# Kernel optimization log

Measured on AMD Instinct MI355X. Metric: run time of the kernel, lower is better.

Reference implementation:

```python
import jax, jax.numpy as jnp
import numpy as np

EPS = 1e-5  # torch BatchNorm1d default eps

# BinActive: sign forward, straight-through estimator backward (grad clipped where |x|>1)
@jax.custom_vjp
def bin_active(x):
    return jnp.sign(x)

def _ba_fwd(x):
    return jnp.sign(x), x

def _ba_bwd(x, g):
    return (g * (jnp.abs(x) <= 1.0).astype(g.dtype),)

bin_active.defvjp(_ba_fwd, _ba_bwd)

# XNOR-style weight binarization: sign(W) * mean(|W|) per output column, STE backward
@jax.custom_vjp
def bin_weight(w):
    alpha = jnp.mean(jnp.abs(w), axis=0, keepdims=True)  # [1, out]
    return jnp.sign(w) * alpha

def _bw_fwd(w):
    alpha = jnp.mean(jnp.abs(w), axis=0, keepdims=True)
    return jnp.sign(w) * alpha, w

def _bw_bwd(w, g):
    return (g * (jnp.abs(w) <= 1.0).astype(g.dtype),)

bin_weight.defvjp(_bw_fwd, _bw_bwd)


def setup_inputs() -> dict:
    key = jax.random.key(0)
    ks = jax.random.split(key, 8)
    N, E, IN, H, OUT = 100000, 1600000, 256, 128, 40
    x = jax.random.normal(ks[0], (N, IN), dtype=jnp.float32)
    edge_index = jax.random.randint(ks[1], (2, E), 0, N, dtype=jnp.int64)
    W0 = jax.random.normal(ks[2], (IN, H), dtype=jnp.float32) * (2.0 / IN) ** 0.5
    b0 = jnp.zeros((H,), dtype=jnp.float32)
    W1 = jax.random.normal(ks[3], (H, H), dtype=jnp.float32) * (2.0 / H) ** 0.5
    b1 = jnp.zeros((H,), dtype=jnp.float32)
    W2 = jax.random.normal(ks[4], (H, OUT), dtype=jnp.float32) * (2.0 / H) ** 0.5
    b2 = jnp.zeros((OUT,), dtype=jnp.float32)
    return {"x": x, "edge_index": edge_index, "W0": W0, "b0": b0,
            "W1": W1, "b1": b1, "W2": W2, "b2": b2}


def reference(x, edge_index, W0, b0, W1, b1, W2, b2):
    n = x.shape[0]
    loop = jnp.arange(n, dtype=edge_index.dtype)
    src = jnp.concatenate([edge_index[0], loop])  # add self loops (GCN norm)
    dst = jnp.concatenate([edge_index[1], loop])
    deg = jax.ops.segment_sum(jnp.ones_like(src, dtype=x.dtype), dst, num_segments=n)
    dinv = jnp.where(deg > 0, deg ** -0.5, 0.0)
    norm = (dinv[src] * dinv[dst])[:, None]  # [E+N, 1]

    # BatchNorm1d(affine=False), training-mode batch statistics (biased var)
    mu = jnp.mean(x, axis=0)
    var = jnp.var(x, axis=0)
    h = (x - mu) * jax.lax.rsqrt(var + EPS)

    for W, b in ((W0, b0), (W1, b1), (W2, b2)):
        h = bin_active(h)                       # sign binarize (dropout skipped: eval)
        h = h @ bin_weight(W)                   # binary-weight linear
        h = jax.ops.segment_sum(h[src] * norm, dst, num_segments=n) + b  # D^-1/2 (A+I) D^-1/2 agg
    return jax.nn.log_softmax(h, axis=1)
```

## Files before the change

### kernel.cpp

```cpp
#include <hip/hip_runtime.h>
#include <math.h>

#define IN_DIM 256
#define HD 128
#define OUT_DIM 40
#define S2_STRIDE 64
#define NB_CS 1024
#define NXCD 8
#define NCHUNK 64
#define NRANGE 8
#define RMAXW 6400

__device__ __forceinline__ int xcc_id() {
    int x;
    asm volatile("s_getreg_b32 %0, hwreg(HW_REG_XCC_ID)" : "=s"(x));
    return x & (NXCD - 1);
}

__global__ __launch_bounds__(256) void k_init(float* muacc8) {
    int i = blockIdx.x * 256 + threadIdx.x;
    if (i < NXCD * 256) muacc8[i] = 0.f;
}

__global__ __launch_bounds__(256) void k_fuse1(const float* __restrict__ x, int N,
                                               float* __restrict__ muacc8,
                                               const int* __restrict__ ei, int E,
                                               unsigned char* __restrict__ cntC,
                                               const float* __restrict__ W0,
                                               const float* __restrict__ W1,
                                               const float* __restrict__ W2,
                                               unsigned long long* W0p,
                                               unsigned long long* W1p,
                                               unsigned long long* W2p,
                                               float* aS0, float* aS1, float* aS2) {
    __shared__ __align__(16) unsigned ldsbuf[RMAXW];
    int b = blockIdx.x, tid = threadIdx.x;
    if (b < NB_CS) {
        float* lds = (float*)ldsbuf;
        size_t F4 = (size_t)N * (IN_DIM / 4);
        size_t stride = (size_t)NB_CS * 256;
        float a0 = 0.f, a1 = 0.f, a2 = 0.f, a3 = 0.f;
        const float4* x4 = (const float4*)x;
        for (size_t i = (size_t)b * 256 + tid; i < F4; i += stride) {
            float4 v = x4[i];
            a0 += v.x; a1 += v.y; a2 += v.z; a3 += v.w;
        }
        lds[tid] = 0.f;
        __syncthreads();
        int c0 = (tid * 4) & 255;
        atomicAdd(&lds[c0], a0);
        atomicAdd(&lds[c0 + 1], a1);
        atomicAdd(&lds[c0 + 2], a2);
        atomicAdd(&lds[c0 + 3], a3);
        __syncthreads();
        int xc = xcc_id();
        __hip_atomic_fetch_add(&muacc8[xc * 256 + tid], lds[tid],
                               __ATOMIC_RELAXED, __HIP_MEMORY_SCOPE_WORKGROUP);
    } else if (b < NB_CS + NCHUNK * NRANGE) {
        int bid2 = b - NB_CS;
        int c = bid2 >> 3, r = bid2 & (NRANGE - 1);
        for (int i = tid; i < RMAXW; i += 256) ldsbuf[i] = 0u;
        __syncthreads();
        int R = (N + NRANGE - 1) / NRANGE;
        int base = r * R;
        int lim = N - base; if (lim > R) lim = R; if (lim < 0) lim = 0;
        int chunk = ((E + NCHUNK - 1) / NCHUNK + 3) & ~3;
        int eBeg = c * chunk, eEnd = E < eBeg + chunk ? E : eBeg + chunk;
        const int* dptr = ei + E;
        int e = eBeg;
        if ((((unsigned)(E + eBeg)) & 3u) == 0 && eBeg < eEnd) {
            int n4 = (eEnd - eBeg) >> 2;
            const int4* d4 = (const int4*)(dptr + eBeg);
            for (int i = tid; i < n4; i += 256) {
                int4 v = d4[i];
                unsigned r0 = (unsigned)(v.x - base);
                unsigned r1 = (unsigned)(v.y - base);
                unsigned r2 = (unsigned)(v.z - base);
                unsigned r3 = (unsigned)(v.w - base);
                if (r0 < (unsigned)lim) atomicAdd(&ldsbuf[r0 >> 1], 1u << (16 * (r0 & 1)));
                if (r1 < (unsigned)lim) atomicAdd(&ldsbuf[r1 >> 1], 1u << (16 * (r1 & 1)));
                if (r2 < (unsigned)lim) atomicAdd(&ldsbuf[r2 >> 1], 1u << (16 * (r2 & 1)));
                if (r3 < (unsigned)lim) atomicAdd(&ldsbuf[r3 >> 1], 1u << (16 * (r3 & 1)));
            }
            e = eBeg + (n4 << 2);
        }
        for (e += tid; e < eEnd; e += 256) {
            unsigned rel = (unsigned)(dptr[e] - base);
            if (rel < (unsigned)lim) atomicAdd(&ldsbuf[rel >> 1], 1u << (16 * (rel & 1)));
        }
        __syncthreads();
        for (int i = tid; i < lim; i += 256) {
            unsigned cv = (ldsbuf[i >> 1] >> (16 * (i & 1))) & 0xFFFFu;
            cntC[(size_t)c * N + base + i] = (unsigned char)cv;
        }
    } else {
        int b2 = b - NB_CS - NCHUNK * NRANGE;
        int lane = tid & 63, w = tid >> 6;
        if (b2 < 32) {
            int j = b2 * 4 + w;
            float asum = 0.f;
            unsigned long long words[4];
            #pragma unroll
            for (int q = 0; q < 4; ++q) {
                float v = W0[(size_t)(4 * lane + q) * HD + j];
                asum += fabsf(v);
                words[q] = __ballot(v < 0.f);
            }
            #pragma unroll
            for (int off = 32; off; off >>= 1) asum += __shfl_xor(asum, off);
            if (lane == 0) {
                aS0[j] = 2.f * asum / 256.f;
                #pragma unroll
                for (int q = 0; q < 4; ++q) W0p[j * 4 + q] = words[q];
            }
        } else if (b2 < 64) {
            int j = (b2 - 32) * 4 + w;
            int fl = lane & 15, kk = lane >> 4;
            float asum = 0.f;
            unsigned long long words[2];
            #pragma unroll
            for (int q = 0; q < 2; ++q) {
                float v = W1[(size_t)(fl * 8 + 4 * q + kk) * HD + j];
                asum += fabsf(v);
                words[q] = __ballot(v < 0.f);
            }
            #pragma unroll
            for (int off = 32; off; off >>= 1) asum += __shfl_xor(asum, off);
            if (lane == 0) {
                aS1[j] = 2.f * asum / 128.f;
                W1p[j * 2 + 0] = words[0];
                W1p[j * 2 + 1] = words[1];
            }
        } else {
            int j = (b2 - 64) * 4 + w;
            int fl = lane & 15, kk = lane >> 4;
            if (j < OUT_DIM) {
                float asum = 0.f;
                unsigned long long words[2];
                #pragma unroll
                for (int q = 0; q < 2; ++q) {
                    float v = W2[(size_t)(fl * 8 + 4 * q + kk) * OUT_DIM + j];
                    asum += fabsf(v);
                    words[q] = __ballot(v < 0.f);
                }
                #pragma unroll
                for (int off = 32; off; off >>= 1) asum += __shfl_xor(asum, off);
                if (lane == 0) {
                    aS2[j] = 2.f * asum / 128.f;
                    W2p[j * 2 + 0] = words[0];
                    W2p[j * 2 + 1] = words[1];
                }
            }
        }
    }
}

__global__ __launch_bounds__(256) void k_bp(unsigned char* __restrict__ cntC, int N,
                                            int* bp, float* __restrict__ dinv,
                                            int* __restrict__ cnt) {
    __shared__ int sm[256];
    int i = blockIdx.x * 256 + threadIdx.x;
    int c = 0;
    if (i < N) {
        int run = 0;
        #pragma unroll
        for (int h = 0; h < NCHUNK; ++h) {
            unsigned bc = cntC[(size_t)h * N + i];
            cntC[(size_t)h * N + i] = (unsigned char)run;
            run += (int)bc;
        }
        c = run;
        cnt[i] = run;
        dinv[i] = (float)(1.0 / sqrt((double)(run + 1)));
    }
    sm[threadIdx.x] = c;
    __syncthreads();
    for (int off = 128; off; off >>= 1) {
        if (threadIdx.x < off) sm[threadIdx.x] += sm[threadIdx.x + off];
        __syncthreads();
    }
    if (threadIdx.x == 0) bp[blockIdx.x] = sm[0];
}

__global__ __launch_bounds__(512) void k_scanbp(const int* __restrict__ bp, int NB, int* bps,
                                                const float* __restrict__ muacc8,
                                                float* __restrict__ mu) {
    __shared__ int sm[512];
    int t = threadIdx.x;
    if (t < 256) {
        float s = 0.f;
        #pragma unroll
        for (int xc = 0; xc < NXCD; ++xc) s += muacc8[xc * 256 + t];
        mu[t] = s;
    }
    int v = (t < NB) ? bp[t] : 0;
    sm[t] = v;
    __syncthreads();
    for (int off = 1; off < 512; off <<= 1) {
        int add = (t >= off) ? sm[t - off] : 0;
        __syncthreads();
        sm[t] += add;
        __syncthreads();
    }
    if (t < NB) bps[t] = sm[t] - v;
}

__global__ __launch_bounds__(256) void k_rowptr(const int* __restrict__ cnt,
                                                const int* __restrict__ bps, int N, int E,
                                                int* row_ptr) {
    __shared__ int wsum[4];
    int t = threadIdx.x, lane = t & 63, w = t >> 6;
    int i = blockIdx.x * 256 + t;
    int c = (i < N) ? cnt[i] : 0;
    int v = c;
    #pragma unroll
    for (int off = 1; off < 64; off <<= 1) {
        int n = __shfl_up(v, off);
        if (lane >= off) v += n;
    }
    if (lane == 63) wsum[w] = v;
    __syncthreads();
    int wo = 0;
    for (int k = 0; k < w; ++k) wo += wsum[k];
    int excl = bps[blockIdx.x] + wo + v - c;
    if (i < N) row_ptr[i] = excl;
    if (blockIdx.x == 0 && t == 0) row_ptr[N] = E;
}

__global__ __launch_bounds__(256) void k_fuse2(const int* __restrict__ ei, int E,
                                               const int* __restrict__ rowp,
                                               const unsigned char* __restrict__ xoffC,
                                               int* __restrict__ cs4,
                                               const float* __restrict__ x,
                                               const float* __restrict__ muacc, float inv_n,
                                               const unsigned long long* __restrict__ W0p,
                                               unsigned char* __restrict__ S0, int N) {
    __shared__ __align__(16) unsigned sh32[RMAXW];
    int b = blockIdx.x, tid = threadIdx.x;
    if (b < NCHUNK * NRANGE) {
        int c = b >> 3, r = b & (NRANGE - 1);
        for (int i = tid; i < RMAXW; i += 256) sh32[i] = 0u;
        __syncthreads();
        int R = (N + NRANGE - 1) / NRANGE;
        int base = r * R;
        int lim = N - base; if (lim > R) lim = R; if (lim < 0) lim = 0;
        int chunk = ((E + NCHUNK - 1) / NCHUNK + 3) & ~3;
        int eBeg = c * chunk, eEnd = E < eBeg + chunk ? E : eBeg + chunk;
        int e = eBeg;
        if (((unsigned)eBeg & 3u) == 0 && (((unsigned)(E + eBeg)) & 3u) == 0 && eBeg < eEnd) {
            int n4 = (eEnd - eBeg) >> 2;
            const int4* s4p = (const int4*)(ei + eBeg);
            const int4* d4p = (const int4*)(ei + E + eBeg);
            for (int i = tid; i < n4; i += 256) {
                int4 sv = s4p[i];
                int4 dv = d4p[i];
                int ss[4] = {sv.x, sv.y, sv.z, sv.w};
                int dd[4] = {dv.x, dv.y, dv.z, dv.w};
                #pragma unroll
                for (int k = 0; k < 4; ++k) {
                    unsigned rel = (unsigned)(dd[k] - base);
                    if (rel < (unsigned)lim) {
                        unsigned old = atomicAdd(&sh32[rel >> 1], 1u << (16 * (rel & 1)));
                        int lr = (int)((old >> (16 * (rel & 1))) & 0xFFFFu);
                        int pos = rowp[dd[k]] +
                                  (int)xoffC[(size_t)c * N + dd[k]] + lr;
                        cs4[pos] = ss[k];
                    }
                }
            }
            e = eBeg + (n4 << 2);
        }
        for (e += tid; e < eEnd; e += 256) {
            int d = ei[E + e];
            unsigned rel = (unsigned)(d - base);
            if (rel < (unsigned)lim) {
                unsigned old = atomicAdd(&sh32[rel >> 1], 1u << (16 * (rel & 1)));
                int lr = (int)((old >> (16 * (rel & 1))) & 0xFFFFu);
                int pos = rowp[d] + (int)xoffC[(size_t)c * N + d] + lr;
                cs4[pos] = ei[e];
            }
        }
    } else {
        unsigned long long* w0s = (unsigned long long*)sh32;
        {
            int i = tid;
            w0s[9 * (i >> 3) + (i & 7)] = W0p[i];
            i = tid + 256;
            w0s[9 * (i >> 3) + (i & 7)] = W0p[i];
        }
        __syncthreads();
        int lane = tid & 63;
        int row = (b - NCHUNK * NRANGE) * 4 + (tid >> 6);
        if (row >= N) return;
        float4 xv = ((const float4*)(x + (size_t)row * IN_DIM))[lane];
        float4 ms = ((const float4*)muacc)[lane];
        unsigned long long xw[4];
        xw[0] = __ballot(xv.x < ms.x * inv_n);
        xw[1] = __ballot(xv.y < ms.y * inv_n);
        xw[2] = __ballot(xv.z < ms.z * inv_n);
        xw[3] = __ballot(xv.w < ms.w * inv_n);
        unsigned int pack = 0;
        #pragma unroll
        for (int t2 = 0; t2 < 2; ++t2) {
            const unsigned long long* wc = &w0s[9 * lane + 4 * t2];
            int dd = __popcll(xw[0] ^ wc[0]) + __popcll(xw[1] ^ wc[1]) +
                     __popcll(xw[2] ^ wc[2]) + __popcll(xw[3] ^ wc[3]);
            int S = IN_DIM - 2 * dd;
            int s8 = S >> 1;
            if (s8 > 127) s8 = 127;
            pack |= ((unsigned int)(s8 + 128) & 0xffu) << (8 * t2);
        }
        *(unsigned short*)(S0 + (size_t)row * HD + 2 * lane) = (unsigned short)pack;
    }
}

__device__ __forceinline__ void acc4s(float n, unsigned v, float* a) {
    a[0] = fmaf(n, (float)(v & 0xffu) - 128.f, a[0]);
    a[1] = fmaf(n, (float)((v >> 8) & 0xffu) - 128.f, a[1]);
    a[2] = fmaf(n, (float)((v >> 16) & 0xffu) - 128.f, a[2]);
    a[3] = fmaf(n, (float)(v >> 24) - 128.f, a[3]);
}

template <int OUTC>
__global__ __launch_bounds__(256) void k_agg_mm(const unsigned char* __restrict__ Sin,
                                                const int* __restrict__ row_ptr,
                                                const int* __restrict__ cs4,
                                                const float* __restrict__ dinv,
                                                const float* __restrict__ alphaS,
                                                const float* __restrict__ bias,
                                                const unsigned long long* __restrict__ Wnp,
                                                unsigned char* __restrict__ Sout, int N) {
    __shared__ unsigned long long wsm[OUTC * 2 + OUTC / 4 + 8];
    int tid = threadIdx.x;
    for (int i = tid; i < OUTC * 2; i += 256) wsm[9 * (i >> 3) + (i & 7)] = Wnp[i];
    __syncthreads();
    int lane = tid & 63;
    int d = blockIdx.x * 4 + (tid >> 6);
    if (d >= N) return;
    int sub = lane >> 4;
    int fl  = lane & 15;
    float dv = dinv[d];
    float acc[8];
    #pragma unroll
    for (int k = 0; k < 8; ++k) acc[k] = 0.f;
    if (sub == 0) {
        float nrm = dv * dv;
        unsigned long long rr = *(const unsigned long long*)(Sin + (size_t)d * HD + fl * 8);
        acc4s(nrm, (unsigned)rr, acc);
        acc4s(nrm, (unsigned)(rr >> 32), acc + 4);
    }
    int e0 = row_ptr[d], e1 = row_ptr[d + 1];
    int e = e0 + sub;
    for (; e + 12 < e1; e += 16) {
        int s0_ = cs4[e], s1_ = cs4[e + 4], s2_ = cs4[e + 8], s3_ = cs4[e + 12];
        float n0 = dinv[s0_] * dv, n1 = dinv[s1_] * dv;
        float n2 = dinv[s2_] * dv, n3 = dinv[s3_] * dv;
        unsigned long long r0 = *(const unsigned long long*)(Sin + (size_t)s0_ * HD + fl * 8);
        unsigned long long r1 = *(const unsigned long long*)(Sin + (size_t)s1_ * HD + fl * 8);
        unsigned long long r2 = *(const unsigned long long*)(Sin + (size_t)s2_ * HD + fl * 8);
        unsigned long long r3 = *(const unsigned long long*)(Sin + (size_t)s3_ * HD + fl * 8);
        acc4s(n0, (unsigned)r0, acc); acc4s(n0, (unsigned)(r0 >> 32), acc + 4);
        acc4s(n1, (unsigned)r1, acc); acc4s(n1, (unsigned)(r1 >> 32), acc + 4);
        acc4s(n2, (unsigned)r2, acc); acc4s(n2, (unsigned)(r2 >> 32), acc + 4);
        acc4s(n3, (unsigned)r3, acc); acc4s(n3, (unsigned)(r3 >> 32), acc + 4);
    }
    for (; e + 4 < e1; e += 8) {
        int sa = cs4[e], sb = cs4[e + 4];
        float na = dinv[sa] * dv, nb = dinv[sb] * dv;
        unsigned long long ra = *(const unsigned long long*)(Sin + (size_t)sa * HD + fl * 8);
        unsigned long long rb = *(const unsigned long long*)(Sin + (size_t)sb * HD + fl * 8);
        acc4s(na, (unsigned)ra, acc); acc4s(na, (unsigned)(ra >> 32), acc + 4);
        acc4s(nb, (unsigned)rb, acc); acc4s(nb, (unsigned)(rb >> 32), acc + 4);
    }
    if (e < e1) {
        int s = cs4[e];
        float nrm = dinv[s] * dv;
        unsigned long long rr = *(const unsigned long long*)(Sin + (size_t)s * HD + fl * 8);
        acc4s(nrm, (unsigned)rr, acc);
        acc4s(nrm, (unsigned)(rr >> 32), acc + 4);
    }
    #pragma unroll
    for (int k = 0; k < 8; ++k) {
        acc[k] += __shfl_xor(acc[k], 16);
        acc[k] += __shfl_xor(acc[k], 32);
    }
    unsigned int m8 = 0;
    #pragma unroll
    for (int k = 0; k < 8; ++k) {
        int f = fl * 8 + k;
        float v = alphaS[f] * acc[k] + bias[f];
        if (v < 0.f) m8 |= (1u << k);
    }
    unsigned long long x0 = 0, x1 = 0;
    #pragma unroll
    for (int k = 0; k < 4; ++k) {
        unsigned long long bk = __ballot((m8 >> k) & 1u);
        x0 |= (bk & 0xffffULL) << (16 * k);
    }
    #pragma unroll
    for (int k = 4; k < 8; ++k) {
        unsigned long long bk = __ballot((m8 >> k) & 1u);
        x1 |= (bk & 0xffffULL) << (16 * (k - 4));
    }
    if (OUTC == 128) {
        unsigned int pack = 0;
        #pragma unroll
        for (int t2 = 0; t2 < 2; ++t2) {
            int j = 2 * lane + t2;
            int i0 = j * 2;
            const unsigned long long* wc = &wsm[9 * (i0 >> 3) + (i0 & 7)];
            int dd = __popcll(x0 ^ wc[0]) + __popcll(x1 ^ wc[1]);
            int S = HD - 2 * dd;
            pack |= ((unsigned int)((S >> 1) + 128) & 0xffu) << (8 * t2);
        }
        *(unsigned short*)(Sout + (size_t)d * HD + 2 * lane) = (unsigned short)pack;
    } else {
        int p8 = 128;
        if (lane < OUTC) {
            int i0 = lane * 2;
            const unsigned long long* wc = &wsm[9 * (i0 >> 3) + (i0 & 7)];
            int dd = __popcll(x0 ^ wc[0]) + __popcll(x1 ^ wc[1]);
            p8 = ((HD - 2 * dd) >> 1) + 128;
        }
        Sout[(size_t)d * S2_STRIDE + lane] = (unsigned char)p8;
    }
}

__global__ __launch_bounds__(256) void k_agg_out(const unsigned char* __restrict__ S2,
                                                 const int* __restrict__ row_ptr,
                                                 const int* __restrict__ cs4,
                                                 const float* __restrict__ dinv,
                                                 const float* __restrict__ alphaS2,
                                                 const float* __restrict__ b2,
                                                 float* __restrict__ out, int N) {
    int tid = threadIdx.x, lane = tid & 63;
    int d = blockIdx.x * 4 + (tid >> 6);
    if (d >= N) return;
    int sub = lane >> 4;
    int fl  = lane & 15;
    float dv = dinv[d];
    float acc[4] = {0.f, 0.f, 0.f, 0.f};
    if (sub == 0) {
        float nrm = dv * dv;
        unsigned int r4 = *(const unsigned int*)(S2 + (size_t)d * S2_STRIDE + fl * 4);
        acc4s(nrm, r4, acc);
    }
    int e0 = row_ptr[d], e1 = row_ptr[d + 1];
    int e = e0 + sub;
    for (; e + 12 < e1; e += 16) {
        int s0_ = cs4[e], s1_ = cs4[e + 4], s2_ = cs4[e + 8], s3_ = cs4[e + 12];
        float n0 = dinv[s0_] * dv, n1 = dinv[s1_] * dv;
        float n2 = dinv[s2_] * dv, n3 = dinv[s3_] * dv;
        unsigned int r0 = *(const unsigned int*)(S2 + (size_t)s0_ * S2_STRIDE + fl * 4);
        unsigned int r1 = *(const unsigned int*)(S2 + (size_t)s1_ * S2_STRIDE + fl * 4);
        unsigned int r2 = *(const unsigned int*)(S2 + (size_t)s2_ * S2_STRIDE + fl * 4);
        unsigned int r3 = *(const unsigned int*)(S2 + (size_t)s3_ * S2_STRIDE + fl * 4);
        acc4s(n0, r0, acc);
        acc4s(n1, r1, acc);
        acc4s(n2, r2, acc);
        acc4s(n3, r3, acc);
    }
    for (; e + 4 < e1; e += 8) {
        int sa = cs4[e], sb = cs4[e + 4];
        float na = dinv[sa] * dv, nb = dinv[sb] * dv;
        unsigned int ra = *(const unsigned int*)(S2 + (size_t)sa * S2_STRIDE + fl * 4);
        unsigned int rb = *(const unsigned int*)(S2 + (size_t)sb * S2_STRIDE + fl * 4);
        acc4s(na, ra, acc);
        acc4s(nb, rb, acc);
    }
    if (e < e1) {
        int s = cs4[e];
        float nrm = dinv[s] * dv;
        unsigned int r4 = *(const unsigned int*)(S2 + (size_t)s * S2_STRIDE + fl * 4);
        acc4s(nrm, r4, acc);
    }
    #pragma unroll
    for (int k = 0; k < 4; ++k) {
        acc[k] += __shfl_xor(acc[k], 16);
        acc[k] += __shfl_xor(acc[k], 32);
    }
    float h[4];
    float mymax = -INFINITY;
    #pragma unroll
    for (int k = 0; k < 4; ++k) {
        int f = fl * 4 + k;
        h[k] = (f < OUT_DIM) ? (alphaS2[f] * acc[k] + b2[f]) : -INFINITY;
        mymax = fmaxf(mymax, h[k]);
    }
    #pragma unroll
    for (int off = 1; off < 16; off <<= 1) mymax = fmaxf(mymax, __shfl_xor(mymax, off));
    float s4 = 0.f;
    #pragma unroll
    for (int k = 0; k < 4; ++k) {
        if (fl * 4 + k < OUT_DIM) s4 += expf(h[k] - mymax);
    }
    #pragma unroll
    for (int off = 1; off < 16; off <<= 1) s4 += __shfl_xor(s4, off);
    float lse = mymax + logf(s4);
    if (sub == 0 && fl < OUT_DIM / 4) {
        float4 o;
        o.x = h[0] - lse; o.y = h[1] - lse; o.z = h[2] - lse; o.w = h[3] - lse;
        *(float4*)(out + (size_t)d * OUT_DIM + fl * 4) = o;
    }
}

extern "C" void kernel_launch(void* const* d_in, const int* in_sizes, int n_in,
                              void* d_out, int out_size, void* d_ws, size_t ws_size,
                              hipStream_t stream) {
    const float* x  = (const float*)d_in[0];
    const int*   ei = (const int*)d_in[1];
    const float* W0 = (const float*)d_in[2];
    const float* b0 = (const float*)d_in[3];
    const float* W1 = (const float*)d_in[4];
    const float* b1 = (const float*)d_in[5];
    const float* W2 = (const float*)d_in[6];
    const float* b2 = (const float*)d_in[7];
    float* out = (float*)d_out;

    int N = in_sizes[0] / IN_DIM;
    int E = in_sizes[1] / 2;

    char* ws = (char*)d_ws;
    size_t off = 0;
    auto alloc = [&](size_t bytes) -> void* {
        off = (off + 255) & ~(size_t)255;
        void* p = (void*)(ws + off);
        off += bytes;
        return p;
    };
    float* mu     = (float*)alloc(256 * 4);
    float* muacc8 = (float*)alloc(NXCD * 256 * 4);
    unsigned char* cntC = (unsigned char*)alloc((size_t)NCHUNK * N);
    int*   cnt    = (int*)alloc((size_t)N * 4);
    float* dinv   = (float*)alloc((size_t)N * 4);
    int*   rowp   = (int*)alloc(((size_t)N + 1) * 4);
    int*   bp     = (int*)alloc(512 * 4);
    int*   bps    = (int*)alloc(512 * 4);
    int*   cs4    = (int*)alloc((size_t)E * 4);
    unsigned char* S0 = (unsigned char*)alloc((size_t)N * HD);
    unsigned char* S1 = (unsigned char*)alloc((size_t)N * HD);
    unsigned char* S2 = (unsigned char*)alloc((size_t)N * S2_STRIDE);
    unsigned long long* W0p = (unsigned long long*)alloc(128 * 4 * 8);
    unsigned long long* W1p = (unsigned long long*)alloc(128 * 2 * 8);
    unsigned long long* W2p = (unsigned long long*)alloc(40 * 2 * 8);
    float* aS0 = (float*)alloc(128 * 4);
    float* aS1 = (float*)alloc(128 * 4);
    float* aS2 = (float*)alloc(40 * 4);

    int nb256 = (N + 255) / 256;
    float inv_n = 1.0f / (float)N;

    k_init<<<dim3(8), dim3(256), 0, stream>>>(muacc8);
    k_fuse1<<<dim3(NB_CS + NCHUNK * NRANGE + 74), dim3(256), 0, stream>>>(
        x, N, muacc8, ei, E, cntC, W0, W1, W2, W0p, W1p, W2p, aS0, aS1, aS2);
    k_bp<<<dim3(nb256), dim3(256), 0, stream>>>(cntC, N, bp, dinv, cnt);
    k_scanbp<<<dim3(1), dim3(512), 0, stream>>>(bp, nb256, bps, muacc8, mu);
    k_rowptr<<<dim3(nb256), dim3(256), 0, stream>>>(cnt, bps, N, E, rowp);

    int nb4 = (N + 3) / 4;
    k_fuse2<<<dim3(NCHUNK * NRANGE + nb4), dim3(256), 0, stream>>>(
        ei, E, rowp, cntC, cs4, x, mu, inv_n, W0p, S0, N);
    k_agg_mm<128><<<dim3(nb4), dim3(256), 0, stream>>>(S0, rowp, cs4, dinv, aS0, b0, W1p, S1, N);
    k_agg_mm<40><<<dim3(nb4), dim3(256), 0, stream>>>(S1, rowp, cs4, dinv, aS1, b1, W2p, S2, N);
    k_agg_out<<<dim3(nb4), dim3(256), 0, stream>>>(S2, rowp, cs4, dinv, aS2, b2, out, N);
    (void)out_size; (void)ws_size; (void)n_in;
}
```

Baseline: 458.8 us.

## Pack degree counters as bytes, use fewer ranges, restructure gather lanes per feature

The degree-counting and CSR-scatter phases now pack four 8-bit counters per LDS word, so each block covers half the node range and only two range blocks per edge chunk are needed. This cuts how many times the destination array is re-read. Edge-index loads switch to nontemporal loads. The hidden and output aggregation kernels change from four sub-groups of 16 lanes, each reading wide rows, to a full wave with one lane per feature pair. Each lane walks every edge with 8-way unrolling, which removes the cross-subgroup shuffle reductions but issues narrower, more numerous gather loads. The 8-bit counters assume per-chunk in-degree stays under 256. W1 and W2 bit packing is reordered to match the new lane-to-feature mapping.

New measurement: 555.2 us. 1.21x slower.

```diff
diff --git a/kernel.cpp b/kernel.cpp
--- a/kernel.cpp
+++ b/kernel.cpp
@@ -8,13 +8,20 @@
 #define NB_CS 1024
 #define NXCD 8
 #define NCHUNK 64
-#define NRANGE 8
-#define RMAXW 6400
+#define NRANGE 2
+#define RMAXW 12800
 
 __device__ __forceinline__ int xcc_id() {
     int x;
     asm volatile("s_getreg_b32 %0, hwreg(HW_REG_XCC_ID)" : "=s"(x));
     return x & (NXCD - 1);
+}
+
+__device__ __forceinline__ void nt_load4(const int* p, int* o) {
+    o[0] = __builtin_nontemporal_load(p + 0);
+    o[1] = __builtin_nontemporal_load(p + 1);
+    o[2] = __builtin_nontemporal_load(p + 2);
+    o[3] = __builtin_nontemporal_load(p + 3);
 }
 
 __global__ __launch_bounds__(256) void k_init(float* muacc8) {
@@ -58,7 +65,7 @@
                                __ATOMIC_RELAXED, __HIP_MEMORY_SCOPE_WORKGROUP);
     } else if (b < NB_CS + NCHUNK * NRANGE) {
         int bid2 = b - NB_CS;
-        int c = bid2 >> 3, r = bid2 & (NRANGE - 1);
+        int c = bid2 >> 1, r = bid2 & (NRANGE - 1);
         for (int i = tid; i < RMAXW; i += 256) ldsbuf[i] = 0u;
         __syncthreads();
         int R = (N + NRANGE - 1) / NRANGE;
@@ -70,27 +77,27 @@
         int e = eBeg;
         if ((((unsigned)(E + eBeg)) & 3u) == 0 && eBeg < eEnd) {
             int n4 = (eEnd - eBeg) >> 2;
-            const int4* d4 = (const int4*)(dptr + eBeg);
             for (int i = tid; i < n4; i += 256) {
-                int4 v = d4[i];
-                unsigned r0 = (unsigned)(v.x - base);
-                unsigned r1 = (unsigned)(v.y - base);
-                unsigned r2 = (unsigned)(v.z - base);
-                unsigned r3 = (unsigned)(v.w - base);
-                if (r0 < (unsigned)lim) atomicAdd(&ldsbuf[r0 >> 1], 1u << (16 * (r0 & 1)));
-                if (r1 < (unsigned)lim) atomicAdd(&ldsbuf[r1 >> 1], 1u << (16 * (r1 & 1)));
-                if (r2 < (unsigned)lim) atomicAdd(&ldsbuf[r2 >> 1], 1u << (16 * (r2 & 1)));
-                if (r3 < (unsigned)lim) atomicAdd(&ldsbuf[r3 >> 1], 1u << (16 * (r3 & 1)));
+                int dd[4];
+                nt_load4(dptr + eBeg + 4 * i, dd);
+                unsigned r0 = (unsigned)(dd[0] - base);
+                unsigned r1 = (unsigned)(dd[1] - base);
+                unsigned r2 = (unsigned)(dd[2] - base);
+                unsigned r3 = (unsigned)(dd[3] - base);
+                if (r0 < (unsigned)lim) atomicAdd(&ldsbuf[r0 >> 2], 1u << (8 * (r0 & 3)));
+                if (r1 < (unsigned)lim) atomicAdd(&ldsbuf[r1 >> 2], 1u << (8 * (r1 & 3)));
+                if (r2 < (unsigned)lim) atomicAdd(&ldsbuf[r2 >> 2], 1u << (8 * (r2 & 3)));
+                if (r3 < (unsigned)lim) atomicAdd(&ldsbuf[r3 >> 2], 1u << (8 * (r3 & 3)));
             }
             e = eBeg + (n4 << 2);
         }
         for (e += tid; e < eEnd; e += 256) {
             unsigned rel = (unsigned)(dptr[e] - base);
-            if (rel < (unsigned)lim) atomicAdd(&ldsbuf[rel >> 1], 1u << (16 * (rel & 1)));
+            if (rel < (unsigned)lim) atomicAdd(&ldsbuf[rel >> 2], 1u << (8 * (rel & 3)));
         }
         __syncthreads();
         for (int i = tid; i < lim; i += 256) {
-            unsigned cv = (ldsbuf[i >> 1] >> (16 * (i & 1))) & 0xFFFFu;
+            unsigned cv = (ldsbuf[i >> 2] >> (8 * (i & 3))) & 0xFFu;
             cntC[(size_t)c * N + base + i] = (unsigned char)cv;
         }
     } else {
@@ -115,14 +122,13 @@
             }
         } else if (b2 < 64) {
             int j = (b2 - 32) * 4 + w;
-            int fl = lane & 15, kk = lane >> 4;
             float asum = 0.f;
             unsigned long long words[2];
             #pragma unroll
-            for (int q = 0; q < 2; ++q) {
-                float v = W1[(size_t)(fl * 8 + 4 * q + kk) * HD + j];
+            for (int p = 0; p < 2; ++p) {
+                float v = W1[(size_t)(2 * lane + p) * HD + j];
                 asum += fabsf(v);
-                words[q] = __ballot(v < 0.f);
+                words[p] = __ballot(v < 0.f);
             }
             #pragma unroll
             for (int off = 32; off; off >>= 1) asum += __shfl_xor(asum, off);
@@ -133,15 +139,14 @@
             }
         } else {
             int j = (b2 - 64) * 4 + w;
-            int fl = lane & 15, kk = lane >> 4;
             if (j < OUT_DIM) {
                 float asum = 0.f;
                 unsigned long long words[2];
                 #pragma unroll
-                for (int q = 0; q < 2; ++q) {
-                    float v = W2[(size_t)(fl * 8 + 4 * q + kk) * OUT_DIM + j];
+                for (int p = 0; p < 2; ++p) {
+                    float v = W2[(size_t)(2 * lane + p) * OUT_DIM + j];
                     asum += fabsf(v);
-                    words[q] = __ballot(v < 0.f);
+                    words[p] = __ballot(v < 0.f);
                 }
                 #pragma unroll
                 for (int off = 32; off; off >>= 1) asum += __shfl_xor(asum, off);
@@ -238,7 +243,7 @@
     __shared__ __align__(16) unsigned sh32[RMAXW];
     int b = blockIdx.x, tid = threadIdx.x;
     if (b < NCHUNK * NRANGE) {
-        int c = b >> 3, r = b & (NRANGE - 1);
+        int c = b >> 1, r = b & (NRANGE - 1);
         for (int i = tid; i < RMAXW; i += 256) sh32[i] = 0u;
         __syncthreads();
         int R = (N + NRANGE - 1) / NRANGE;
@@ -249,19 +254,16 @@
         int e = eBeg;
         if (((unsigned)eBeg & 3u) == 0 && (((unsigned)(E + eBeg)) & 3u) == 0 && eBeg < eEnd) {
             int n4 = (eEnd - eBeg) >> 2;
-            const int4* s4p = (const int4*)(ei + eBeg);
-            const int4* d4p = (const int4*)(ei + E + eBeg);
             for (int i = tid; i < n4; i += 256) {
-                int4 sv = s4p[i];
-                int4 dv = d4p[i];
-                int ss[4] = {sv.x, sv.y, sv.z, sv.w};
-                int dd[4] = {dv.x, dv.y, dv.z, dv.w};
+                int ss[4], dd[4];
+                nt_load4(ei + eBeg + 4 * i, ss);
+                nt_load4(ei + E + eBeg + 4 * i, dd);
                 #pragma unroll
                 for (int k = 0; k < 4; ++k) {
                     unsigned rel = (unsigned)(dd[k] - base);
                     if (rel < (unsigned)lim) {
-                        unsigned old = atomicAdd(&sh32[rel >> 1], 1u << (16 * (rel & 1)));
-                        int lr = (int)((old >> (16 * (rel & 1))) & 0xFFFFu);
+                        unsigned old = atomicAdd(&sh32[rel >> 2], 1u << (8 * (rel & 3)));
+                        int lr = (int)((old >> (8 * (rel & 3))) & 0xFFu);
                         int pos = rowp[dd[k]] +
                                   (int)xoffC[(size_t)c * N + dd[k]] + lr;
                         cs4[pos] = ss[k];
@@ -274,8 +276,8 @@
             int d = ei[E + e];
             unsigned rel = (unsigned)(d - base);
             if (rel < (unsigned)lim) {
-                unsigned old = atomicAdd(&sh32[rel >> 1], 1u << (16 * (rel & 1)));
-                int lr = (int)((old >> (16 * (rel & 1))) & 0xFFFFu);
+                unsigned old = atomicAdd(&sh32[rel >> 2], 1u << (8 * (rel & 3)));
+                int lr = (int)((old >> (8 * (rel & 3))) & 0xFFu);
                 int pos = rowp[d] + (int)xoffC[(size_t)c * N + d] + lr;
                 cs4[pos] = ei[e];
             }
@@ -312,13 +314,6 @@
         }
         *(unsigned short*)(S0 + (size_t)row * HD + 2 * lane) = (unsigned short)pack;
     }
-}
-
-__device__ __forceinline__ void acc4s(float n, unsigned v, float* a) {
-    a[0] = fmaf(n, (float)(v & 0xffu) - 128.f, a[0]);
-    a[1] = fmaf(n, (float)((v >> 8) & 0xffu) - 128.f, a[1]);
-    a[2] = fmaf(n, (float)((v >> 16) & 0xffu) - 128.f, a[2]);
-    a[3] = fmaf(n, (float)(v >> 24) - 128.f, a[3]);
 }
 
 template <int OUTC>
@@ -337,73 +332,48 @@
     int lane = tid & 63;
     int d = blockIdx.x * 4 + (tid >> 6);
     if (d >= N) return;
-    int sub = lane >> 4;
-    int fl  = lane & 15;
+    unsigned fo = (unsigned)lane * 2;
     float dv = dinv[d];
-    float acc[8];
-    #pragma unroll
-    for (int k = 0; k < 8; ++k) acc[k] = 0.f;
-    if (sub == 0) {
+    float p0a[4] = {0.f, 0.f, 0.f, 0.f};
+    float p1a[4] = {0.f, 0.f, 0.f, 0.f};
+    {
         float nrm = dv * dv;
-        unsigned long long rr = *(const unsigned long long*)(Sin + (size_t)d * HD + fl * 8);
-        acc4s(nrm, (unsigned)rr, acc);
-        acc4s(nrm, (unsigned)(rr >> 32), acc + 4);
+        unsigned v = *(const unsigned short*)(Sin + (((unsigned)d << 7) + fo));
+        p0a[0] = fmaf(nrm, (float)(v & 0xffu) - 128.f, p0a[0]);
+        p1a[0] = fmaf(nrm, (float)(v >> 8) - 128.f, p1a[0]);
     }
     int e0 = row_ptr[d], e1 = row_ptr[d + 1];
-    int e = e0 + sub;
-    for (; e + 12 < e1; e += 16) {
-        int s0_ = cs4[e], s1_ = cs4[e + 4], s2_ = cs4[e + 8], s3_ = cs4[e + 12];
-        float n0 = dinv[s0_] * dv, n1 = dinv[s1_] * dv;
-        float n2 = dinv[s2_] * dv, n3 = dinv[s3_] * dv;
-        unsigned long long r0 = *(const unsigned long long*)(Sin + (size_t)s0_ * HD + fl * 8);
-        unsigned long long r1 = *(const unsigned long long*)(Sin + (size_t)s1_ * HD + fl * 8);
-        unsigned long long r2 = *(const unsigned long long*)(Sin + (size_t)s2_ * HD + fl * 8);
-        unsigned long long r3 = *(const unsigned long long*)(Sin + (size_t)s3_ * HD + fl * 8);
-        acc4s(n0, (unsigned)r0, acc); acc4s(n0, (unsigned)(r0 >> 32), acc + 4);
-        acc4s(n1, (unsigned)r1, acc); acc4s(n1, (unsigned)(r1 >> 32), acc + 4);
-        acc4s(n2, (unsigned)r2, acc); acc4s(n2, (unsigned)(r2 >> 32), acc + 4);
-        acc4s(n3, (unsigned)r3, acc); acc4s(n3, (unsigned)(r3 >> 32), acc + 4);
-    }
-    for (; e + 4 < e1; e += 8) {
-        int sa = cs4[e], sb = cs4[e + 4];
-        float na = dinv[sa] * dv, nb = dinv[sb] * dv;
-        unsigned long long ra = *(const unsigned long long*)(Sin + (size_t)sa * HD + fl * 8);
-        unsigned long long rb = *(const unsigned long long*)(Sin + (size_t)sb * HD + fl * 8);
-        acc4s(na, (unsigned)ra, acc); acc4s(na, (unsigned)(ra >> 32), acc + 4);
-        acc4s(nb, (unsigned)rb, acc); acc4s(nb, (unsigned)(rb >> 32), acc + 4);
-    }
-    if (e < e1) {
+    int e = e0;
+    for (; e + 7 < e1; e += 8) {
+        int s[8]; float n[8]; unsigned v[8];
+        #pragma unroll
+        for (int j = 0; j < 8; ++j) s[j] = __builtin_nontemporal_load(&cs4[e + j]);
+        #pragma unroll
+        for (int j = 0; j < 8; ++j) n[j] = dinv[s[j]] * dv;
+        #pragma unroll
+        for (int j = 0; j < 8; ++j)
+            v[j] = *(const unsigned short*)(Sin + (((unsigned)s[j] << 7) + fo));
+        #pragma unroll
+        for (int j = 0; j < 8; ++j) {
+            p0a[j & 3] = fmaf(n[j], (float)(v[j] & 0xffu) - 128.f, p0a[j & 3]);
+            p1a[j & 3] = fmaf(n[j], (float)(v[j] >> 8) - 128.f, p1a[j & 3]);
+        }
+    }
+    for (int q = 0; e < e1; ++e, ++q) {
         int s = cs4[e];
         float nrm = dinv[s] * dv;
-        unsigned long long rr = *(const unsigned long long*)(Sin + (size_t)s * HD + fl * 8);
-        acc4s(nrm, (unsigned)rr, acc);
-        acc4s(nrm, (unsigned)(rr >> 32), acc + 4);
-    }
-    #pragma unroll
-    for (int k = 0; k < 8; ++k) {
-        acc[k] += __shfl_xor(acc[k], 16);
-        acc[k] += __shfl_xor(acc[k], 32);
-    }
-    unsigned int m8 = 0;
-    #pragma unroll
-    for (int k = 0; k < 8; ++k) {
-        int f = fl * 8 + k;
-        float v = alphaS[f] * acc[k] + bias[f];
-        if (v < 0.f) m8 |= (1u << k);
-    }
-    unsigned long long x0 = 0, x1 = 0;
-    #pragma unroll
-    for (int k = 0; k < 4; ++k) {
-        unsigned long long bk = __ballot((m8 >> k) & 1u);
-        x0 |= (bk & 0xffffULL) << (16 * k);
-    }
-    #pragma unroll
-    for (int k = 4; k < 8; ++k) {
-        unsigned long long bk = __ballot((m8 >> k) & 1u);
-        x1 |= (bk & 0xffffULL) << (16 * (k - 4));
-    }
+        unsigned v = *(const unsigned short*)(Sin + (((unsigned)s << 7) + fo));
+        p0a[q & 3] = fmaf(nrm, (float)(v & 0xffu) - 128.f, p0a[q & 3]);
+        p1a[q & 3] = fmaf(nrm, (float)(v >> 8) - 128.f, p1a[q & 3]);
+    }
+    float a0 = (p0a[0] + p0a[1]) + (p0a[2] + p0a[3]);
+    float a1 = (p1a[0] + p1a[1]) + (p1a[2] + p1a[3]);
+    float h0 = alphaS[fo] * a0 + bias[fo];
+    float h1 = alphaS[fo + 1] * a1 + bias[fo + 1];
+    unsigned long long x0 = __ballot(h0 < 0.f);
+    unsigned long long x1 = __ballot(h1 < 0.f);
     if (OUTC == 128) {
-        unsigned int pack = 0;
+        unsigned pack = 0;
         #pragma unroll
         for (int t2 = 0; t2 < 2; ++t2) {
             int j = 2 * lane + t2;
@@ -411,9 +381,9 @@
             const unsigned long long* wc = &wsm[9 * (i0 >> 3) + (i0 & 7)];
             int dd = __popcll(x0 ^ wc[0]) + __popcll(x1 ^ wc[1]);
             int S = HD - 2 * dd;
-            pack |= ((unsigned int)((S >> 1) + 128) & 0xffu) << (8 * t2);
-        }
-        *(unsigned short*)(Sout + (size_t)d * HD + 2 * lane) = (unsigned short)pack;
+            pack |= ((unsigned)((S >> 1) + 128) & 0xffu) << (8 * t2);
+        }
+        *(unsigned short*)(Sout + (size_t)d * HD + fo) = (unsigned short)pack;
     } else {
         int p8 = 128;
         if (lane < OUTC) {
@@ -436,72 +406,42 @@
     int tid = threadIdx.x, lane = tid & 63;
     int d = blockIdx.x * 4 + (tid >> 6);
     if (d >= N) return;
-    int sub = lane >> 4;
-    int fl  = lane & 15;
     float dv = dinv[d];
-    float acc[4] = {0.f, 0.f, 0.f, 0.f};
-    if (sub == 0) {
+    float pa[4] = {0.f, 0.f, 0.f, 0.f};
+    {
         float nrm = dv * dv;
-        unsigned int r4 = *(const unsigned int*)(S2 + (size_t)d * S2_STRIDE + fl * 4);
-        acc4s(nrm, r4, acc);
+        unsigned v = S2[((unsigned)d << 6) + lane];
+        pa[0] = fmaf(nrm, (float)v - 128.f, pa[0]);
     }
     int e0 = row_ptr[d], e1 = row_ptr[d + 1];
-    int e = e0 + sub;
-    for (; e + 12 < e1; e += 16) {
-        int s0_ = cs4[e], s1_ = cs4[e + 4], s2_ = cs4[e + 8], s3_ = cs4[e + 12];
-        float n0 = dinv[s0_] * dv, n1 = dinv[s1_] * dv;
-        float n2 = dinv[s2_] * dv, n3 = dinv[s3_] * dv;
-        unsigned int r0 = *(const unsigned int*)(S2 + (size_t)s0_ * S2_STRIDE + fl * 4);
-        unsigned int r1 = *(const unsigned int*)(S2 + (size_t)s1_ * S2_STRIDE + fl * 4);
-        unsigned int r2 = *(const unsigned int*)(S2 + (size_t)s2_ * S2_STRIDE + fl * 4);
-        unsigned int r3 = *(const unsigned int*)(S2 + (size_t)s3_ * S2_STRIDE + fl * 4);
-        acc4s(n0, r0, acc);
-        acc4s(n1, r1, acc);
-        acc4s(n2, r2, acc);
-        acc4s(n3, r3, acc);
-    }
-    for (; e + 4 < e1; e += 8) {
-        int sa = cs4[e], sb = cs4[e + 4];
-        float na = dinv[sa] * dv, nb = dinv[sb] * dv;
-        unsigned int ra = *(const unsigned int*)(S2 + (size_t)sa * S2_STRIDE + fl * 4);
-        unsigned int rb = *(const unsigned int*)(S2 + (size_t)sb * S2_STRIDE + fl * 4);
-        acc4s(na, ra, acc);
-        acc4s(nb, rb, acc);
-    }
-    if (e < e1) {
+    int e = e0;
+    for (; e + 7 < e1; e += 8) {
+        int s[8]; float n[8]; unsigned v[8];
+        #pragma unroll
+        for (int j = 0; j < 8; ++j) s[j] = __builtin_nontemporal_load(&cs4[e + j]);
+        #pragma unroll
+        for (int j = 0; j < 8; ++j) n[j] = dinv[s[j]] * dv;
+        #pragma unroll
+        for (int j = 0; j < 8; ++j) v[j] = S2[((unsigned)s[j] << 6) + lane];
+        #pragma unroll
+        for (int j = 0; j < 8; ++j) pa[j & 3] = fmaf(n[j], (float)v[j] - 128.f, pa[j & 3]);
+    }
+    for (int q = 0; e < e1; ++e, ++q) {
         int s = cs4[e];
         float nrm = dinv[s] * dv;
-        unsigned int r4 = *(const unsigned int*)(S2 + (size_t)s * S2_STRIDE + fl * 4);
-        acc4s(nrm, r4, acc);
-    }
+        unsigned v = S2[((unsigned)s << 6) + lane];
+        pa[q & 3] = fmaf(nrm, (float)v - 128.f, pa[q & 3]);
+    }
+    float a0 = (pa[0] + pa[1]) + (pa[2] + pa[3]);
+    float h = (lane < OUT_DIM) ? (alphaS2[lane] * a0 + b2[lane]) : -INFINITY;
+    float mymax = h;
     #pragma unroll
-    for (int k = 0; k < 4; ++k) {
-        acc[k] += __shfl_xor(acc[k], 16);
-        acc[k] += __shfl_xor(acc[k], 32);
-    }
-    float h[4];
-    float mymax = -INFINITY;
+    for (int off = 1; off < 64; off <<= 1) mymax = fmaxf(mymax, __shfl_xor(mymax, off));
+    float s4 = (lane < OUT_DIM) ? expf(h - mymax) : 0.f;
     #pragma unroll
-    for (int k = 0; k < 4; ++k) {
-        int f = fl * 4 + k;
-        h[k] = (f < OUT_DIM) ? (alphaS2[f] * acc[k] + b2[f]) : -INFINITY;
-        mymax = fmaxf(mymax, h[k]);
-    }
-    #pragma unroll
-    for (int off = 1; off < 16; off <<= 1) mymax = fmaxf(mymax, __shfl_xor(mymax, off));
-    float s4 = 0.f;
-    #pragma unroll
-    for (int k = 0; k < 4; ++k) {
-        if (fl * 4 + k < OUT_DIM) s4 += expf(h[k] - mymax);
-    }
-    #pragma unroll
-    for (int off = 1; off < 16; off <<= 1) s4 += __shfl_xor(s4, off);
+    for (int off = 1; off < 64; off <<= 1) s4 += __shfl_xor(s4, off);
     float lse = mymax + logf(s4);
-    if (sub == 0 && fl < OUT_DIM / 4) {
-        float4 o;
-        o.x = h[0] - lse; o.y = h[1] - lse; o.z = h[2] - lse; o.w = h[3] - lse;
-        *(float4*)(out + (size_t)d * OUT_DIM + fl * 4) = o;
-    }
+    if (lane < OUT_DIM) out[(size_t)d * OUT_DIM + lane] = h - lse;
 }
 
 extern "C" void kernel_launch(void* const* d_in, const int* in_sizes, int n_in,
```
